# Performance work log

Hardware: AMD Instinct MI355X
Metric: run time of the kernel (lower is better)

Reference implementation:

```python
import jax, jax.numpy as jnp
import numpy as np


def setup_inputs() -> dict:
    key = jax.random.key(0)
    k1, k2, k3 = jax.random.split(key, 3)
    B, C, H, W = 16, 512, 64, 64
    x = jax.random.normal(k1, (B, C, H, W), dtype=jnp.float32)
    w1 = jax.random.normal(k2, (2 * C // 16, 2 * C), dtype=jnp.float32) * 0.02
    b1 = jnp.zeros((2 * C // 16,), dtype=jnp.float32)
    w2 = jax.random.normal(k3, (C, 2 * C // 16), dtype=jnp.float32) * 0.02
    b2 = jnp.zeros((C,), dtype=jnp.float32)
    return {"x": x, "w1": w1, "b1": b1, "w2": w2, "b2": b2}


def reference(x, w1, b1, w2, b2):
    B, C, H, W = x.shape
    q = x.reshape(B, C, H * W)                       # [B, C, N]
    # channel-channel energy: [B, C, C]
    energy = jnp.einsum('bcn,bdn->bcd', q, q)
    energy_new = jnp.max(energy, axis=-1, keepdims=True) - energy
    attention = jax.nn.softmax(energy_new, axis=-1)  # [B, C, C]
    out = jnp.einsum('bcd,bdn->bcn', attention, q).reshape(B, C, H, W)
    # SE gating on concat([x, out]) -> global avg pool -> 1x1 convs
    pooled = jnp.concatenate([x, out], axis=1).mean(axis=(2, 3))  # [B, 2C]
    h = jax.nn.relu(pooled @ w1.T + b1)                           # [B, 2C//16]
    se = jax.nn.sigmoid(h @ w2.T + b2)[:, :, None, None]          # [B, C, 1, 1]
    return se * x + (1.0 - se) * out
```

## Files before the change

kernel.cpp:

```cpp
#include <hip/hip_runtime.h>
#include <cstdint>
#include <cstddef>

#define BB 16
#define CC 512
#define NN 4096

typedef __attribute__((ext_vector_type(4))) float f32x4;
typedef __attribute__((ext_vector_type(8))) _Float16 f16x8;

#define VMCNT(n) asm volatile("s_waitcnt vmcnt(" #n ")" ::: "memory")

__device__ __forceinline__ unsigned short f2h(float f) {
  _Float16 h = (_Float16)f;
  return __builtin_bit_cast(unsigned short, h);
}
__device__ __forceinline__ float h2f(unsigned short u) {
  return (float)__builtin_bit_cast(_Float16, u);
}
__device__ __forceinline__ unsigned int pk2(float a, float b) {
  return (unsigned int)f2h(a) | ((unsigned int)f2h(b) << 16);
}

__device__ __forceinline__ void gload16(const unsigned short* g, short* l) {
  __builtin_amdgcn_global_load_lds(
      (const __attribute__((address_space(1))) unsigned int*)g,
      (__attribute__((address_space(3))) unsigned int*)(__attribute__((address_space(3))) short*)l,
      16, 0, 0);
}

__global__ __launch_bounds__(256) void k_convert(
    const float* __restrict__ x,
    unsigned short* __restrict__ qh,
    unsigned short* __restrict__ qt,
    float* __restrict__ part)
{
  const int nt = blockIdx.x;
  const int ct = blockIdx.y;
  const int b  = blockIdx.z;
  const int c0 = ct << 6;
  const int n0 = nt << 7;
  const int t  = threadIdx.x;
  const int w  = t >> 6;
  const int l  = t & 63;

  __shared__ unsigned short lt[128 * 65];
  __shared__ float fs[64];

  const size_t xb = (size_t)b * CC * NN;
  const int n8 = (l & 15) << 3;

  #pragma unroll
  for (int i = 0; i < 4; ++i) {
    const int r = (i << 4) + (w << 2) + (l >> 4);
    const size_t off = xb + (size_t)(c0 + r) * NN + n0 + n8;
    const float4 v0 = *(const float4*)(x + off);
    const float4 v1 = *(const float4*)(x + off + 4);
    uint4 pkv;
    pkv.x = pk2(v0.x, v0.y);
    pkv.y = pk2(v0.z, v0.w);
    pkv.z = pk2(v1.x, v1.y);
    pkv.w = pk2(v1.z, v1.w);
    *(uint4*)(qh + off) = pkv;
    lt[(n8 + 0) * 65 + r] = (unsigned short)(pkv.x & 0xffff);
    lt[(n8 + 1) * 65 + r] = (unsigned short)(pkv.x >> 16);
    lt[(n8 + 2) * 65 + r] = (unsigned short)(pkv.y & 0xffff);
    lt[(n8 + 3) * 65 + r] = (unsigned short)(pkv.y >> 16);
    lt[(n8 + 4) * 65 + r] = (unsigned short)(pkv.z & 0xffff);
    lt[(n8 + 5) * 65 + r] = (unsigned short)(pkv.z >> 16);
    lt[(n8 + 6) * 65 + r] = (unsigned short)(pkv.w & 0xffff);
    lt[(n8 + 7) * 65 + r] = (unsigned short)(pkv.w >> 16);
    float s = (v0.x + v0.y) + (v0.z + v0.w) + (v1.x + v1.y) + (v1.z + v1.w);
    s += __shfl_xor(s, 1);
    s += __shfl_xor(s, 2);
    s += __shfl_xor(s, 4);
    s += __shfl_xor(s, 8);
    if ((l & 15) == 0) fs[r] = s;
  }
  __syncthreads();
  if (t < 64) part[((size_t)b * CC + c0 + t) * 32 + nt] = fs[t];

  #pragma unroll
  for (int p = 0; p < 4; ++p) {
    const int n   = (p << 5) + (t >> 3);
    const int cc8 = (t & 7) << 3;
    const unsigned short* e = &lt[n * 65 + cc8];
    uint4 pk;
    pk.x = (unsigned)e[0] | ((unsigned)e[1] << 16);
    pk.y = (unsigned)e[2] | ((unsigned)e[3] << 16);
    pk.z = (unsigned)e[4] | ((unsigned)e[5] << 16);
    pk.w = (unsigned)e[6] | ((unsigned)e[7] << 16);
    *(uint4*)(qt + ((size_t)b * NN + n0 + n) * CC + c0 + cc8) = pk;
  }
}

__global__ __launch_bounds__(256) void k_sumpart(const float* __restrict__ part,
                                                 float* __restrict__ px)
{
  const int g = blockIdx.x * 256 + threadIdx.x;
  float s = 0.f;
  #pragma unroll
  for (int i = 0; i < 32; ++i) s += part[(size_t)g * 32 + i];
  px[g] = s;
}

template <int KSPLIT>
__global__ __launch_bounds__(256, 3) void k_energy(
    const unsigned short* __restrict__ qh,
    float* __restrict__ EP)
{
  const int bx  = blockIdx.x;
  const int xcd = bx & 7;
  const int j   = bx >> 3;
  const int gi  = j / 10;
  const int t10 = j % 10;
  const int g   = xcd + (gi << 3);
  const int b   = g / KSPLIT;
  const int ks  = g % KSPLIT;
  int tr, tc;
  if (t10 < 4)      { tr = 0; tc = t10; }
  else if (t10 < 7) { tr = 1; tc = t10 - 3; }
  else if (t10 < 9) { tr = 2; tc = t10 - 5; }
  else              { tr = 3; tc = 3; }
  const bool diag = (tr == tc);
  const int kbase = ks * (NN / KSPLIT);
  const int NK    = 128 / KSPLIT;

  const int t = threadIdx.x, w = t >> 6, l = t & 63;
  const int wr = w >> 1, wc = w & 1;

  __shared__ short lds[3][2][128 * 32];

  const size_t qoff = (size_t)b * CC * NN;
  const unsigned short* sA = qh + qoff + (size_t)(tr * 128) * NN;
  const unsigned short* sB = diag ? sA : qh + qoff + (size_t)(tc * 128) * NN;

  const int r1 = w * 16 + (l >> 2);
  const int kl = (((l & 3) ^ (l >> 4)) << 3);
  const int d1 = w * 512;
  const int d2 = 2048 + w * 512;
  const int laneoff = ((l & 15) << 5) + ((((l >> 4) ^ ((l >> 2) & 3))) << 3);

  f32x4 acc[4][4] = {};

  auto stage = [&](int buf, int kk) {
    const int k0 = kbase + kk * 32 + kl;
    gload16(sA + (size_t)r1 * NN + k0,        &lds[buf][0][d1]);
    gload16(sA + (size_t)(r1 + 64) * NN + k0, &lds[buf][0][d2]);
    gload16(sB + (size_t)r1 * NN + k0,        &lds[buf][1][d1]);
    gload16(sB + (size_t)(r1 + 64) * NN + k0, &lds[buf][1][d2]);
  };

  stage(0, 0);
  stage(1, 1);
  VMCNT(4);
  __builtin_amdgcn_s_barrier();

  for (int kk = 0; kk < NK; ++kk) {
    const int cur = kk % 3;
    if (kk + 2 < NK) stage((kk + 2) % 3, kk + 2);
    const short* A = &lds[cur][0][0];
    const short* Bm = &lds[cur][1][0];
    f16x8 ah[4], bh[4];
    #pragma unroll
    for (int m = 0; m < 4; ++m)
      ah[m] = *(const f16x8*)(A + (wr * 64 + m * 16) * 32 + laneoff);
    #pragma unroll
    for (int n = 0; n < 4; ++n)
      bh[n] = *(const f16x8*)(Bm + (wc * 64 + n * 16) * 32 + laneoff);
    __builtin_amdgcn_s_setprio(1);
    #pragma unroll
    for (int m = 0; m < 4; ++m)
      #pragma unroll
      for (int n = 0; n < 4; ++n)
        acc[m][n] = __builtin_amdgcn_mfma_f32_16x16x32_f16(ah[m], bh[n], acc[m][n], 0, 0, 0);
    __builtin_amdgcn_s_setprio(0);
    if (kk + 2 < NK)      VMCNT(4);
    else if (kk + 1 < NK) VMCNT(0);
    __builtin_amdgcn_s_barrier();
  }

  const int row0 = tr * 128 + wr * 64, col0 = tc * 128 + wc * 64;
  float* Eb = EP + ((size_t)ks * BB + b) * CC * CC;
  #pragma unroll
  for (int m = 0; m < 4; ++m)
    #pragma unroll
    for (int n = 0; n < 4; ++n)
      #pragma unroll
      for (int r = 0; r < 4; ++r) {
        const int row = row0 + m * 16 + ((l >> 4) << 2) + r;
        const int col = col0 + n * 16 + (l & 15);
        const float v = acc[m][n][r];
        Eb[(size_t)row * CC + col] = v;
        if (!diag) Eb[(size_t)col * CC + row] = v;
      }
}

template <int NP>
__global__ __launch_bounds__(64) void k_softmax(
    const float* __restrict__ EP, const float* __restrict__ px,
    unsigned short* __restrict__ att, float* __restrict__ po)
{
  const int bx = blockIdx.x;
  const int b = bx >> 9, c = bx & 511;
  const int l = threadIdx.x;
  const size_t row4 = (((size_t)b * CC + c) * CC) >> 2;
  const size_t PS4 = ((size_t)BB * CC * CC) >> 2;
  const float4* E4 = (const float4*)EP;

  float v[8];
  {
    float4 a = E4[row4 + 2 * l];
    float4 bq = E4[row4 + 2 * l + 1];
    #pragma unroll
    for (int p = 1; p < NP; ++p) {
      const float4 a2 = E4[(size_t)p * PS4 + row4 + 2 * l];
      const float4 b2 = E4[(size_t)p * PS4 + row4 + 2 * l + 1];
      a.x += a2.x; a.y += a2.y; a.z += a2.z; a.w += a2.w;
      bq.x += b2.x; bq.y += b2.y; bq.z += b2.z; bq.w += b2.w;
    }
    v[0] = a.x; v[1] = a.y; v[2] = a.z; v[3] = a.w;
    v[4] = bq.x; v[5] = bq.y; v[6] = bq.z; v[7] = bq.w;
  }
  float mn = v[0];
  #pragma unroll
  for (int i = 1; i < 8; ++i) mn = fminf(mn, v[i]);
  #pragma unroll
  for (int o = 32; o > 0; o >>= 1) mn = fminf(mn, __shfl_xor(mn, o));
  float s = 0.f;
  #pragma unroll
  for (int i = 0; i < 8; ++i) { v[i] = __expf(mn - v[i]); s += v[i]; }
  float dot;
  {
    const float4* px4 = (const float4*)(px + (size_t)b * CC);
    const float4 p0 = px4[2 * l];
    const float4 p1 = px4[2 * l + 1];
    dot = v[0] * p0.x + v[1] * p0.y + v[2] * p0.z + v[3] * p0.w
        + v[4] * p1.x + v[5] * p1.y + v[6] * p1.z + v[7] * p1.w;
  }
  #pragma unroll
  for (int o = 32; o > 0; o >>= 1) { s += __shfl_xor(s, o); dot += __shfl_xor(dot, o); }
  const float inv = 1.f / s;
  uint4 pkv;
  pkv.x = pk2(v[0] * inv, v[1] * inv);
  pkv.y = pk2(v[2] * inv, v[3] * inv);
  pkv.z = pk2(v[4] * inv, v[5] * inv);
  pkv.w = pk2(v[6] * inv, v[7] * inv);
  ((uint4*)(att + ((size_t)b * CC + c) * CC))[l] = pkv;
  if (l == 0) po[(size_t)b * CC + c] = dot / (s * 4096.f);
}

__global__ __launch_bounds__(256) void k_mlp(
    const float* __restrict__ px, const float* __restrict__ po,
    const float* __restrict__ w1, const float* __restrict__ b1,
    const float* __restrict__ w2, const float* __restrict__ b2,
    float* __restrict__ se)
{
  const int b = blockIdx.x, t = threadIdx.x;
  __shared__ float p[1024];
  __shared__ float hp[64][5];
  __shared__ float h[64];
  for (int i = t; i < 1024; i += 256)
    p[i] = (i < 512) ? px[(size_t)b * 512 + i] * (1.f / 4096.f)
                     : po[(size_t)b * 512 + i - 512];
  __syncthreads();
  {
    const int j = t >> 2, q = t & 3;
    float s = 0.f;
    const float* wr = w1 + (size_t)j * 1024 + q * 256;
    const float* pp = p + q * 256;
    for (int k = 0; k < 256; ++k) s += pp[k] * wr[k];
    hp[j][q] = s;
  }
  __syncthreads();
  if (t < 64) h[t] = fmaxf(hp[t][0] + hp[t][1] + hp[t][2] + hp[t][3] + b1[t], 0.f);
  __syncthreads();
  for (int c = t; c < 512; c += 256) {
    float s = b2[c];
    for (int j = 0; j < 64; ++j) s += h[j] * w2[(size_t)c * 64 + j];
    se[(size_t)b * 512 + c] = 1.f / (1.f + __expf(-s));
  }
}

__global__ __launch_bounds__(512, 4) void k_out(
    const unsigned short* __restrict__ att,
    const unsigned short* __restrict__ qt,
    const float* __restrict__ se,
    const unsigned short* __restrict__ qh,
    float* __restrict__ out)
{
  const int bx = blockIdx.x;
  const int xcd = bx & 7;
  const int j   = bx >> 3;
  const int b   = xcd + ((j >> 6) << 3);
  const int tt  = j & 63;
  const int tr = tt >> 4, tc = tt & 15;
  const int t = threadIdx.x, w = t >> 6, l = t & 63;
  const int wr = w >> 2, wc = w & 3;

  __shared__ short lds[3][12288];

  const unsigned short* sA = att + (size_t)b * CC * CC + (size_t)(tr * 128) * CC;
  const unsigned short* sB = qt  + (size_t)b * NN * CC + (size_t)(tc * 256) * CC;

  const int r1 = w * 16 + (l >> 2);
  const int kl = (((l & 3) ^ (l >> 4)) << 3);
  const int dA  = w * 512;
  const int dB0 = 4096 + w * 512;
  const int dB1 = 8192 + w * 512;
  const int laneoff = ((l & 15) << 5) + ((((l >> 4) ^ ((l >> 2) & 3))) << 3);

  f32x4 acc[4][4] = {};

  auto stage = [&](int buf, int kk) {
    const int k0 = kk * 32 + kl;
    gload16(sA + (size_t)r1 * CC + k0,         &lds[buf][dA]);
    gload16(sB + (size_t)r1 * CC + k0,         &lds[buf][dB0]);
    gload16(sB + (size_t)(r1 + 128) * CC + k0, &lds[buf][dB1]);
  };

  stage(0, 0);
  stage(1, 1);
  VMCNT(3);
  __builtin_amdgcn_s_barrier();

  for (int kk = 0; kk < 16; ++kk) {
    const int cur = kk % 3;
    if (kk + 2 < 16) stage((kk + 2) % 3, kk + 2);
    const short* A  = &lds[cur][0];
    const short* Bm = &lds[cur][4096];
    f16x8 af[4], bf[4];
    #pragma unroll
    for (int m = 0; m < 4; ++m) af[m] = *(const f16x8*)(A  + (wr * 64 + m * 16) * 32 + laneoff);
    #pragma unroll
    for (int n = 0; n < 4; ++n) bf[n] = *(const f16x8*)(Bm + (wc * 64 + n * 16) * 32 + laneoff);
    __builtin_amdgcn_s_setprio(1);
    #pragma unroll
    for (int m = 0; m < 4; ++m)
      #pragma unroll
      for (int n = 0; n < 4; ++n)
        acc[m][n] = __builtin_amdgcn_mfma_f32_16x16x32_f16(af[m], bf[n], acc[m][n], 0, 0, 0);
    __builtin_amdgcn_s_setprio(0);
    if (kk + 2 < 16)      VMCNT(3);
    else if (kk + 1 < 16) VMCNT(0);
    __builtin_amdgcn_s_barrier();
  }

  float* slab = (float*)(&lds[0][0]) + w * (16 * 68);
  const int row0 = tr * 128 + wr * 64, col0q = tc * 256 + wc * 64;
  const size_t xb = (size_t)b * CC * NN;
  const float* seb = se + (size_t)b * CC;
  #pragma unroll
  for (int m = 0; m < 4; ++m) {
    #pragma unroll
    for (int n = 0; n < 4; ++n)
      #pragma unroll
      for (int r = 0; r < 4; ++r)
        slab[(((l >> 4) << 2) + r) * 68 + n * 16 + (l & 15)] = acc[m][n][r];
    #pragma unroll
    for (int it = 0; it < 4; ++it) {
      const int rl = (it << 2) + (l >> 4);
      const int c  = row0 + m * 16 + rl;
      const int n4 = (l & 15) << 2;
      const float4 a = *(const float4*)&slab[rl * 68 + n4];
      const float sv = seb[c];
      const float om = 1.f - sv;
      const size_t go = xb + (size_t)c * NN + col0q + n4;
      const ushort4 hx = *(const ushort4*)(qh + go);
      float4 o;
      o.x = sv * h2f(hx.x) + om * a.x;
      o.y = sv * h2f(hx.y) + om * a.y;
      o.z = sv * h2f(hx.z) + om * a.z;
      o.w = sv * h2f(hx.w) + om * a.w;
      *(float4*)(out + go) = o;
    }
  }
}

extern "C" void kernel_launch(void* const* d_in, const int* in_sizes, int n_in,
                              void* d_out, int out_size, void* d_ws, size_t ws_size,
                              hipStream_t stream) {
  (void)in_sizes; (void)n_in; (void)out_size;
  const float* x  = (const float*)d_in[0];
  const float* w1 = (const float*)d_in[1];
  const float* b1 = (const float*)d_in[2];
  const float* w2 = (const float*)d_in[3];
  const float* b2 = (const float*)d_in[4];
  float* out = (float*)d_out;

  const size_t O_QH  = 0;
  const size_t O_QT  = 67108864;
  const size_t O_EP  = 134217728;
  const size_t EPSZ1 = 16777216;

  const size_t TAIL = 8388608 + 1048576 + 3 * 32768;
  const size_t NEED1 = O_EP + 1 * EPSZ1 + TAIL;
  const size_t NEED2 = O_EP + 2 * EPSZ1 + TAIL;
  const size_t NEED4 = O_EP + 4 * EPSZ1 + TAIL;

  if (ws_size < NEED1) return;
  const int ksplit = (ws_size >= NEED4) ? 4 : (ws_size >= NEED2) ? 2 : 1;

  char* ws = (char*)d_ws;
  unsigned short* qh  = (unsigned short*)(ws + O_QH);
  unsigned short* qt  = (unsigned short*)(ws + O_QT);
  float*          EP  = (float*)(ws + O_EP);
  char* tail          = ws + O_EP + (size_t)ksplit * EPSZ1;
  unsigned short* att = (unsigned short*)(tail);
  float*          part= (float*)(tail + 8388608);
  float*          px  = (float*)(tail + 9437184);
  float*          po  = (float*)(tail + 9469952);
  float*          se  = (float*)(tail + 9502720);

  k_convert<<<dim3(32, 8, 16), 256, 0, stream>>>(x, qh, qt, part);
  k_sumpart<<<32, 256, 0, stream>>>(part, px);
  if (ksplit == 4) {
    k_energy<4><<<640, 256, 0, stream>>>(qh, EP);
    k_softmax<4><<<8192, 64, 0, stream>>>(EP, px, att, po);
  } else if (ksplit == 2) {
    k_energy<2><<<320, 256, 0, stream>>>(qh, EP);
    k_softmax<2><<<8192, 64, 0, stream>>>(EP, px, att, po);
  } else {
    k_energy<1><<<160, 256, 0, stream>>>(qh, EP);
    k_softmax<1><<<8192, 64, 0, stream>>>(EP, px, att, po);
  }
  k_mlp<<<16, 256, 0, stream>>>(px, po, w1, b1, w2, b2, se);
  k_out<<<1024, 512, 0, stream>>>(att, qt, se, qh, out);
}
```

Before: 214.5 us.

## Drop transposed qt buffer; load B from qh and transpose via ds_read_b64_tr_b16

The convert kernel no longer builds a transposed fp16 copy of x (qt). The output GEMM now loads B tiles directly from the row-major qh layout and uses the LDS transpose-read instruction to form MFMA operands. This removes a 64MB write and the LDS transpose in k_convert. In exchange it adds a full lgkmcnt wait and a sched barrier before the MFMAs, and the B global loads now use a strided access pattern.

```diff
diff --git a/kernel.cpp b/kernel.cpp
--- a/kernel.cpp
+++ b/kernel.cpp
@@ -8,8 +8,12 @@
 
 typedef __attribute__((ext_vector_type(4))) float f32x4;
 typedef __attribute__((ext_vector_type(8))) _Float16 f16x8;
+typedef __attribute__((ext_vector_type(2))) unsigned int u32x2;
+typedef __attribute__((ext_vector_type(4))) unsigned int u32x4;
 
 #define VMCNT(n) asm volatile("s_waitcnt vmcnt(" #n ")" ::: "memory")
+#define TRREAD(dst, p, OFF) \
+  asm volatile("ds_read_b64_tr_b16 %0, %1 offset:" #OFF : "=v"(dst) : "v"(p) : "memory")
 
 __device__ __forceinline__ unsigned short f2h(float f) {
   _Float16 h = (_Float16)f;
@@ -32,7 +36,6 @@
 __global__ __launch_bounds__(256) void k_convert(
     const float* __restrict__ x,
     unsigned short* __restrict__ qh,
-    unsigned short* __restrict__ qt,
     float* __restrict__ part)
 {
   const int nt = blockIdx.x;
@@ -44,7 +47,6 @@
   const int w  = t >> 6;
   const int l  = t & 63;
 
-  __shared__ unsigned short lt[128 * 65];
   __shared__ float fs[64];
 
   const size_t xb = (size_t)b * CC * NN;
@@ -62,14 +64,6 @@
     pkv.z = pk2(v1.x, v1.y);
     pkv.w = pk2(v1.z, v1.w);
     *(uint4*)(qh + off) = pkv;
-    lt[(n8 + 0) * 65 + r] = (unsigned short)(pkv.x & 0xffff);
-    lt[(n8 + 1) * 65 + r] = (unsigned short)(pkv.x >> 16);
-    lt[(n8 + 2) * 65 + r] = (unsigned short)(pkv.y & 0xffff);
-    lt[(n8 + 3) * 65 + r] = (unsigned short)(pkv.y >> 16);
-    lt[(n8 + 4) * 65 + r] = (unsigned short)(pkv.z & 0xffff);
-    lt[(n8 + 5) * 65 + r] = (unsigned short)(pkv.z >> 16);
-    lt[(n8 + 6) * 65 + r] = (unsigned short)(pkv.w & 0xffff);
-    lt[(n8 + 7) * 65 + r] = (unsigned short)(pkv.w >> 16);
     float s = (v0.x + v0.y) + (v0.z + v0.w) + (v1.x + v1.y) + (v1.z + v1.w);
     s += __shfl_xor(s, 1);
     s += __shfl_xor(s, 2);
@@ -79,19 +73,6 @@
   }
   __syncthreads();
   if (t < 64) part[((size_t)b * CC + c0 + t) * 32 + nt] = fs[t];
-
-  #pragma unroll
-  for (int p = 0; p < 4; ++p) {
-    const int n   = (p << 5) + (t >> 3);
-    const int cc8 = (t & 7) << 3;
-    const unsigned short* e = &lt[n * 65 + cc8];
-    uint4 pk;
-    pk.x = (unsigned)e[0] | ((unsigned)e[1] << 16);
-    pk.y = (unsigned)e[2] | ((unsigned)e[3] << 16);
-    pk.z = (unsigned)e[4] | ((unsigned)e[5] << 16);
-    pk.w = (unsigned)e[6] | ((unsigned)e[7] << 16);
-    *(uint4*)(qt + ((size_t)b * NN + n0 + n) * CC + c0 + cc8) = pk;
-  }
 }
 
 __global__ __launch_bounds__(256) void k_sumpart(const float* __restrict__ part,
@@ -284,7 +265,6 @@
 
 __global__ __launch_bounds__(512, 4) void k_out(
     const unsigned short* __restrict__ att,
-    const unsigned short* __restrict__ qt,
     const float* __restrict__ se,
     const unsigned short* __restrict__ qh,
     float* __restrict__ out)
@@ -300,23 +280,28 @@
 
   __shared__ short lds[3][12288];
 
-  const unsigned short* sA = att + (size_t)b * CC * CC + (size_t)(tr * 128) * CC;
-  const unsigned short* sB = qt  + (size_t)b * NN * CC + (size_t)(tc * 256) * CC;
+  const unsigned short* sA  = att + (size_t)b * CC * CC + (size_t)(tr * 128) * CC;
+  const unsigned short* sBq = qh  + (size_t)b * CC * NN;
+  const int n0g = tc * 256;
 
   const int r1 = w * 16 + (l >> 2);
   const int kl = (((l & 3) ^ (l >> 4)) << 3);
-  const int dA  = w * 512;
-  const int dB0 = 4096 + w * 512;
-  const int dB1 = 8192 + w * 512;
+  const int dA = w * 512;
   const int laneoff = ((l & 15) << 5) + ((((l >> 4) ^ ((l >> 2) & 3))) << 3);
 
+  const int sB_s = l >> 3;
+  const int sB_d = ((sB_s & 3) << 3) + ((sB_s >> 2) << 2) + ((l >> 1) & 3);
+  const int sB_n = (l & 1) << 3;
+
+  const int trlane = l << 2;
+
   f32x4 acc[4][4] = {};
 
   auto stage = [&](int buf, int kk) {
-    const int k0 = kk * 32 + kl;
-    gload16(sA + (size_t)r1 * CC + k0,         &lds[buf][dA]);
-    gload16(sB + (size_t)r1 * CC + k0,         &lds[buf][dB0]);
-    gload16(sB + (size_t)(r1 + 128) * CC + k0, &lds[buf][dB1]);
+    gload16(sA + (size_t)r1 * CC + kk * 32 + kl, &lds[buf][dA]);
+    const unsigned short* gB = sBq + (size_t)(kk * 32 + sB_d) * NN + n0g + sB_n;
+    gload16(gB + (2 * w) * 16,     &lds[buf][4096 + (2 * w) * 512]);
+    gload16(gB + (2 * w + 1) * 16, &lds[buf][4096 + (2 * w + 1) * 512]);
   };
 
   stage(0, 0);
@@ -327,13 +312,29 @@
   for (int kk = 0; kk < 16; ++kk) {
     const int cur = kk % 3;
     if (kk + 2 < 16) stage((kk + 2) % 3, kk + 2);
-    const short* A  = &lds[cur][0];
-    const short* Bm = &lds[cur][4096];
+    const short* A = &lds[cur][0];
     f16x8 af[4], bf[4];
     #pragma unroll
-    for (int m = 0; m < 4; ++m) af[m] = *(const f16x8*)(A  + (wr * 64 + m * 16) * 32 + laneoff);
-    #pragma unroll
-    for (int n = 0; n < 4; ++n) bf[n] = *(const f16x8*)(Bm + (wc * 64 + n * 16) * 32 + laneoff);
+    for (int m = 0; m < 4; ++m) af[m] = *(const f16x8*)(A + (wr * 64 + m * 16) * 32 + laneoff);
+    {
+      const __attribute__((address_space(3))) short* p3 =
+          (__attribute__((address_space(3))) short*)&lds[cur][4096 + wc * 2048] + trlane;
+      u32x2 r0, r1v, r2, r3, r4, r5, r6, r7;
+      TRREAD(r0, p3, 0);    TRREAD(r1v, p3, 512);
+      TRREAD(r2, p3, 1024); TRREAD(r3, p3, 1536);
+      TRREAD(r4, p3, 2048); TRREAD(r5, p3, 2560);
+      TRREAD(r6, p3, 3072); TRREAD(r7, p3, 3584);
+      u32x4 c0 = {r0.x, r0.y, r1v.x, r1v.y};
+      u32x4 c1 = {r2.x, r2.y, r3.x, r3.y};
+      u32x4 c2 = {r4.x, r4.y, r5.x, r5.y};
+      u32x4 c3 = {r6.x, r6.y, r7.x, r7.y};
+      bf[0] = __builtin_bit_cast(f16x8, c0);
+      bf[1] = __builtin_bit_cast(f16x8, c1);
+      bf[2] = __builtin_bit_cast(f16x8, c2);
+      bf[3] = __builtin_bit_cast(f16x8, c3);
+    }
+    asm volatile("s_waitcnt lgkmcnt(0)" ::: "memory");
+    __builtin_amdgcn_sched_barrier(0);
     __builtin_amdgcn_s_setprio(1);
     #pragma unroll
     for (int m = 0; m < 4; ++m)
@@ -389,8 +390,7 @@
   float* out = (float*)d_out;
 
   const size_t O_QH  = 0;
-  const size_t O_QT  = 67108864;
-  const size_t O_EP  = 134217728;
+  const size_t O_EP  = 67108864;
   const size_t EPSZ1 = 16777216;
 
   const size_t TAIL = 8388608 + 1048576 + 3 * 32768;
@@ -403,7 +403,6 @@
 
   char* ws = (char*)d_ws;
   unsigned short* qh  = (unsigned short*)(ws + O_QH);
-  unsigned short* qt  = (unsigned short*)(ws + O_QT);
   float*          EP  = (float*)(ws + O_EP);
   char* tail          = ws + O_EP + (size_t)ksplit * EPSZ1;
   unsigned short* att = (unsigned short*)(tail);
@@ -412,7 +411,7 @@
   float*          po  = (float*)(tail + 9469952);
   float*          se  = (float*)(tail + 9502720);
 
-  k_convert<<<dim3(32, 8, 16), 256, 0, stream>>>(x, qh, qt, part);
+  k_convert<<<dim3(32, 8, 16), 256, 0, stream>>>(x, qh, part);
   k_sumpart<<<32, 256, 0, stream>>>(part, px);
   if (ksplit == 4) {
     k_energy<4><<<640, 256, 0, stream>>>(qh, EP);
@@ -425,5 +424,5 @@
     k_softmax<1><<<8192, 64, 0, stream>>>(EP, px, att, po);
   }
   k_mlp<<<16, 256, 0, stream>>>(px, po, w1, b1, w2, b2, se);
-  k_out<<<1024, 512, 0, stream>>>(att, qt, se, qh, out);
-}
+  k_out<<<1024, 512, 0, stream>>>(att, se, qh, out);
+}
```

Result: faster. 184.3 us (-14.1%).
